# Performance work log

Measured on AMD Instinct MI355X. Metric: run time of the kernel, lower is better.

## Reference

```python
import jax, jax.numpy as jnp
import numpy as np

B, N, F_, H, K_IN, K = 2, 768, 128, 128, 2, 2
TAU = 0.66


def setup_inputs() -> dict:
    key = jax.random.key(0)
    ks = jax.random.split(key, 8)
    s = lambda fan: 1.0 / np.sqrt(fan)
    X = jax.random.normal(ks[0], (B, N, F_), jnp.float32)
    # edge_feat RezeroMLP: Linear(F,H) -> act -> Linear(H,H)
    ef_w1 = jax.random.normal(ks[1], (F_, H), jnp.float32) * s(F_)
    ef_b1 = jnp.zeros((H,), jnp.float32)
    ef_w2 = jax.random.normal(ks[2], (H, H), jnp.float32) * s(H)
    ef_b2 = jnp.zeros((H,), jnp.float32)
    # rezero gate (init 0 in module; use small nonzero so the branch is exercised)
    gate = jnp.asarray(0.1, jnp.float32)
    # score_mlp RezeroMLP: Linear(k_in,H) -> ReLU -> Linear(H,k)
    sm_w1 = jax.random.normal(ks[3], (K_IN, H), jnp.float32) * s(K_IN)
    sm_b1 = jnp.zeros((H,), jnp.float32)
    sm_w2 = jax.random.normal(ks[4], (H, K), jnp.float32) * s(H)
    sm_b2 = jnp.zeros((K,), jnp.float32)
    # pre-sampled standard Gumbel noise for gumbel_softmax
    u = jax.random.uniform(ks[5], (B, N, N, K), jnp.float32, minval=1e-6, maxval=1.0 - 1e-6)
    gumbel = -jnp.log(-jnp.log(u))
    return {"X": X, "ef_w1": ef_w1, "ef_b1": ef_b1, "ef_w2": ef_w2, "ef_b2": ef_b2,
            "gate": gate, "sm_w1": sm_w1, "sm_b1": sm_b1, "sm_w2": sm_w2, "sm_b2": sm_b2,
            "gumbel": gumbel}


def reference(X, ef_w1, ef_b1, ef_w2, ef_b2, gate, sm_w1, sm_b1, sm_w2, sm_b2, gumbel):
    # edge_feat MLP: [B,N,F] -> [B,N,H]
    feats = jax.nn.relu(X @ ef_w1 + ef_b1) @ ef_w2 + ef_b2
    D = H // K_IN
    Xact = feats.reshape(B, N, D, K_IN)
    Xskip = X.reshape(B, N, D, K_IN)  # feat_dim == hidden_dim, proj is None
    Xc = (Xskip + gate * Xact).transpose(0, 3, 1, 2)  # [B,k_in,N,D]
    # pairwise outer product ('prod' scoring): [B,N,N,k_in]
    prod = jnp.einsum('bkid,bkjd->bijk', Xc, Xc)
    # per-edge score MLP: k_in -> H -> k
    scores = jax.nn.relu(prod @ sm_w1 + sm_b1) @ sm_w2 + sm_b2  # [B,N,N,k]
    logits = scores - jnp.max(scores, axis=-1, keepdims=True)
    # gumbel-softmax, hard (straight-through)
    y_soft = jax.nn.softmax((logits + gumbel) / TAU, axis=-1)
    y_hard = jax.nn.one_hot(jnp.argmax(y_soft, axis=-1), K, dtype=y_soft.dtype)
    y = y_hard + y_soft - jax.lax.stop_gradient(y_soft)
    # A = y @ zo with zo = [0,1,...]: probability/one-hot mass of 'edge' states
    zo = jnp.ones((K,), y.dtype).at[0].set(0.0)
    A = y @ zo  # [B,N,N]
    # zero diagonal and symmetrize via upper triangle
    Au = jnp.triu(A, 1)
    return Au + jnp.swapaxes(Au, -1, -2)
```

## Files before the change

### kernel.cpp

```cpp
#include <hip/hip_runtime.h>

#define BB 2
#define NN 768
#define FF 128
#define HH 128
#define TS 32
#define ROWS 8

__global__ void pack_weights_kernel(const float* __restrict__ sm_w1,
                                    const float* __restrict__ sm_b1,
                                    const float* __restrict__ sm_w2,
                                    double* __restrict__ wpack) {
    int c = threadIdx.x;
    if (c < HH) {
        wpack[4 * c + 0] = (double)sm_w1[c];
        wpack[4 * c + 1] = (double)sm_w1[HH + c];
        wpack[4 * c + 2] = (double)sm_b1[c];
        wpack[4 * c + 3] = (double)sm_w2[2 * c + 1] - (double)sm_w2[2 * c + 0];
    }
}

__global__ __launch_bounds__(128)
void edgefeat_kernel(const float* __restrict__ X,
                     const float* __restrict__ w1, const float* __restrict__ b1,
                     const float* __restrict__ w2, const float* __restrict__ b2,
                     const float* __restrict__ gatep,
                     double* __restrict__ Xc) {
    __shared__ float  Xs[ROWS][FF];
    __shared__ double Hs[ROWS][HH];
    const int h = threadIdx.x;
    const int row0 = blockIdx.x * ROWS;
    for (int r = 0; r < ROWS; ++r) Xs[r][h] = X[(size_t)(row0 + r) * FF + h];
    __syncthreads();
    double acc[ROWS];
    double bb = (double)b1[h];
    for (int r = 0; r < ROWS; ++r) acc[r] = bb;
    for (int f = 0; f < FF; ++f) {
        double w = (double)w1[f * HH + h];
        for (int r = 0; r < ROWS; ++r) acc[r] = fma((double)Xs[r][f], w, acc[r]);
    }
    for (int r = 0; r < ROWS; ++r) Hs[r][h] = acc[r] > 0.0 ? acc[r] : 0.0;
    __syncthreads();
    bb = (double)b2[h];
    for (int r = 0; r < ROWS; ++r) acc[r] = bb;
    for (int c = 0; c < HH; ++c) {
        double w = (double)w2[c * HH + h];
        for (int r = 0; r < ROWS; ++r) acc[r] = fma(Hs[r][c], w, acc[r]);
    }
    const double gate = (double)gatep[0];
    const int k = h & 1, d = h >> 1;
    const int b = row0 / NN;
    const int i0 = row0 % NN;
    for (int r = 0; r < ROWS; ++r) {
        double v = (double)Xs[r][h] + gate * acc[r];
        Xc[(((size_t)(b * 2 + k)) * NN + (i0 + r)) * 64 + d] = v;
    }
}

__global__ __launch_bounds__(256, 2)
void edge_decide_kernel(const double* __restrict__ Xc,
                        const double* __restrict__ wpack,
                        const float* __restrict__ sm_b2,
                        const float* __restrict__ gumbel,
                        float* __restrict__ out) {
    const int ti = blockIdx.x, tj = blockIdx.y, b = blockIdx.z;
    if (tj < ti) return;
    __shared__ double Ai[2][TS][66];
    __shared__ double Aj[2][TS][66];
    __shared__ float  As[TS][TS + 1];
    const int tid = threadIdx.x;
    const int i0 = ti * TS, j0 = tj * TS;

    for (int q = 0; q < 8; ++q) {
        int flat = tid + 256 * q;
        int k  = flat >> 10;
        int r  = (flat >> 5) & 31;
        int dp = flat & 31;
        size_t base = ((size_t)(b * 2 + k)) * NN;
        double2 vi = *(const double2*)&Xc[(base + i0 + r) * 64 + 2 * dp];
        *(double2*)&Ai[k][r][2 * dp] = vi;
        double2 vj = *(const double2*)&Xc[(base + j0 + r) * 64 + 2 * dp];
        *(double2*)&Aj[k][r][2 * dp] = vj;
    }
    __syncthreads();

    const int rh = tid >> 4;
    const int ch = tid & 15;
    const int r0 = rh, r1 = rh + 16;
    const int c0 = 2 * ch, c1 = c0 + 1;

    double p000 = 0, p001 = 0, p010 = 0, p011 = 0;
    double p100 = 0, p101 = 0, p110 = 0, p111 = 0;
    for (int d2 = 0; d2 < 32; ++d2) {
        double2 a00 = *(const double2*)&Ai[0][r0][2 * d2];
        double2 a01 = *(const double2*)&Ai[0][r1][2 * d2];
        double2 a10 = *(const double2*)&Ai[1][r0][2 * d2];
        double2 a11 = *(const double2*)&Ai[1][r1][2 * d2];
        double2 b00 = *(const double2*)&Aj[0][c0][2 * d2];
        double2 b01 = *(const double2*)&Aj[0][c1][2 * d2];
        double2 b10 = *(const double2*)&Aj[1][c0][2 * d2];
        double2 b11 = *(const double2*)&Aj[1][c1][2 * d2];
        p000 = fma(a00.y, b00.y, fma(a00.x, b00.x, p000));
        p001 = fma(a00.y, b01.y, fma(a00.x, b01.x, p001));
        p010 = fma(a01.y, b00.y, fma(a01.x, b00.x, p010));
        p011 = fma(a01.y, b01.y, fma(a01.x, b01.x, p011));
        p100 = fma(a10.y, b10.y, fma(a10.x, b10.x, p100));
        p101 = fma(a10.y, b11.y, fma(a10.x, b11.x, p101));
        p110 = fma(a11.y, b10.y, fma(a11.x, b10.x, p110));
        p111 = fma(a11.y, b11.y, fma(a11.x, b11.x, p111));
    }

    const double bd = (double)sm_b2[1] - (double)sm_b2[0];
    float4 g0v = *(const float4*)&gumbel[(((size_t)b * NN + i0 + r0) * NN + j0 + c0) * 2];
    float4 g1v = *(const float4*)&gumbel[(((size_t)b * NN + i0 + r1) * NN + j0 + c0) * 2];
    double m00 = bd + ((double)g0v.y - (double)g0v.x);
    double m01 = bd + ((double)g0v.w - (double)g0v.z);
    double m10 = bd + ((double)g1v.y - (double)g1v.x);
    double m11 = bd + ((double)g1v.w - (double)g1v.z);

    for (int c = 0; c < HH; ++c) {
        double2 wab = *(const double2*)&wpack[4 * c];
        double2 wbw = *(const double2*)&wpack[4 * c + 2];
        double t;
        t = fma(p100, wab.y, fma(p000, wab.x, wbw.x)); t = fmax(t, 0.0); m00 = fma(t, wbw.y, m00);
        t = fma(p101, wab.y, fma(p001, wab.x, wbw.x)); t = fmax(t, 0.0); m01 = fma(t, wbw.y, m01);
        t = fma(p110, wab.y, fma(p010, wab.x, wbw.x)); t = fmax(t, 0.0); m10 = fma(t, wbw.y, m10);
        t = fma(p111, wab.y, fma(p011, wab.x, wbw.x)); t = fmax(t, 0.0); m11 = fma(t, wbw.y, m11);
    }

    float A00 = m00 > 0.0 ? 1.0f : 0.0f;
    float A01 = m01 > 0.0 ? 1.0f : 0.0f;
    float A10 = m10 > 0.0 ? 1.0f : 0.0f;
    float A11 = m11 > 0.0 ? 1.0f : 0.0f;

    As[r0][c0] = A00; As[r0][c1] = A01;
    As[r1][c0] = A10; As[r1][c1] = A11;
    __syncthreads();

    if (ti != tj) {
        *(float2*)&out[((size_t)b * NN + i0 + r0) * NN + j0 + c0] = make_float2(A00, A01);
        *(float2*)&out[((size_t)b * NN + i0 + r1) * NN + j0 + c0] = make_float2(A10, A11);
        float2 t0 = make_float2(As[c0][r0], As[c1][r0]);
        *(float2*)&out[((size_t)b * NN + j0 + r0) * NN + i0 + c0] = t0;
        float2 t1 = make_float2(As[c0][r1], As[c1][r1]);
        *(float2*)&out[((size_t)b * NN + j0 + r1) * NN + i0 + c0] = t1;
    } else {
        float v00 = (r0 < c0) ? As[r0][c0] : ((r0 > c0) ? As[c0][r0] : 0.0f);
        float v01 = (r0 < c1) ? As[r0][c1] : ((r0 > c1) ? As[c1][r0] : 0.0f);
        float v10 = (r1 < c0) ? As[r1][c0] : ((r1 > c0) ? As[c0][r1] : 0.0f);
        float v11 = (r1 < c1) ? As[r1][c1] : ((r1 > c1) ? As[c1][r1] : 0.0f);
        *(float2*)&out[((size_t)b * NN + i0 + r0) * NN + j0 + c0] = make_float2(v00, v01);
        *(float2*)&out[((size_t)b * NN + i0 + r1) * NN + j0 + c0] = make_float2(v10, v11);
    }
}

extern "C" void kernel_launch(void* const* d_in, const int* in_sizes, int n_in,
                              void* d_out, int out_size, void* d_ws, size_t ws_size,
                              hipStream_t stream) {
    const float* X      = (const float*)d_in[0];
    const float* ef_w1  = (const float*)d_in[1];
    const float* ef_b1  = (const float*)d_in[2];
    const float* ef_w2  = (const float*)d_in[3];
    const float* ef_b2  = (const float*)d_in[4];
    const float* gate   = (const float*)d_in[5];
    const float* sm_w1  = (const float*)d_in[6];
    const float* sm_b1  = (const float*)d_in[7];
    const float* sm_w2  = (const float*)d_in[8];
    const float* sm_b2  = (const float*)d_in[9];
    const float* gumbel = (const float*)d_in[10];
    float* out = (float*)d_out;

    double* Xc    = (double*)d_ws;
    double* wpack = Xc + (size_t)BB * 2 * NN * 64;

    pack_weights_kernel<<<1, 128, 0, stream>>>(sm_w1, sm_b1, sm_w2, wpack);
    edgefeat_kernel<<<BB * NN / ROWS, 128, 0, stream>>>(X, ef_w1, ef_b1, ef_w2, ef_b2, gate, Xc);
    dim3 grid(NN / TS, NN / TS, BB);
    edge_decide_kernel<<<grid, 256, 0, stream>>>(Xc, wpack, sm_b2, gumbel, out);
}
```

Baseline: 134.2 us.

## Run score MLP in fp32 with fp64 fallback near decision boundary; fuse weight packing

The per-edge 128-wide score MLP now runs in fp32 from a packed float4 weight table. Only when the fp32 margin falls below a small threshold does it recompute that edge in fp64 through a non-inlined helper. This cuts the dominant fp64 FMA cost while keeping exact hard decisions for near-tie edges. The weight-pack kernel is folded into the edge-feature kernel's first block, removing one launch, and ROWS is halved to give that kernel more blocks. The risk is a wrong decision if fp32 error ever exceeds the threshold, plus divergence cost in the rare fallback path.

```diff
diff --git a/kernel.cpp b/kernel.cpp
--- a/kernel.cpp
+++ b/kernel.cpp
@@ -5,19 +5,27 @@
 #define FF 128
 #define HH 128
 #define TS 32
-#define ROWS 8
-
-__global__ void pack_weights_kernel(const float* __restrict__ sm_w1,
-                                    const float* __restrict__ sm_b1,
-                                    const float* __restrict__ sm_w2,
-                                    double* __restrict__ wpack) {
-    int c = threadIdx.x;
-    if (c < HH) {
-        wpack[4 * c + 0] = (double)sm_w1[c];
-        wpack[4 * c + 1] = (double)sm_w1[HH + c];
-        wpack[4 * c + 2] = (double)sm_b1[c];
-        wpack[4 * c + 3] = (double)sm_w2[2 * c + 1] - (double)sm_w2[2 * c + 0];
-    }
+#define ROWS 4
+#define THR 4e-3f
+
+__device__ __attribute__((noinline))
+double mlp_f64(const double* __restrict__ wpack, double p0, double p1, double m) {
+#pragma unroll 1
+    for (int c = 0; c < HH; ++c) {
+        double2 wab = *(const double2*)&wpack[4 * c];
+        double2 wbw = *(const double2*)&wpack[4 * c + 2];
+        double t = fma(p1, wab.y, fma(p0, wab.x, wbw.x));
+        t = fmax(t, 0.0);
+        m = fma(t, wbw.y, m);
+    }
+    return m;
+}
+
+__device__ inline float decide(float m32, double p0, double p1, double init,
+                               const double* __restrict__ wpack) {
+    if (__builtin_expect(fabsf(m32) < THR, 0))
+        return mlp_f64(wpack, p0, p1, init) > 0.0 ? 1.0f : 0.0f;
+    return m32 > 0.0f ? 1.0f : 0.0f;
 }
 
 __global__ __launch_bounds__(128)
@@ -25,12 +33,27 @@
                      const float* __restrict__ w1, const float* __restrict__ b1,
                      const float* __restrict__ w2, const float* __restrict__ b2,
                      const float* __restrict__ gatep,
-                     double* __restrict__ Xc) {
+                     const float* __restrict__ sm_w1, const float* __restrict__ sm_b1,
+                     const float* __restrict__ sm_w2,
+                     double* __restrict__ Xc,
+                     double* __restrict__ wpack,
+                     float4* __restrict__ wpackf) {
     __shared__ float  Xs[ROWS][FF];
     __shared__ double Hs[ROWS][HH];
     const int h = threadIdx.x;
     const int row0 = blockIdx.x * ROWS;
     for (int r = 0; r < ROWS; ++r) Xs[r][h] = X[(size_t)(row0 + r) * FF + h];
+    if (blockIdx.x == 0) {
+        double a  = (double)sm_w1[h];
+        double bq = (double)sm_w1[HH + h];
+        double be = (double)sm_b1[h];
+        double wd = (double)sm_w2[2 * h + 1] - (double)sm_w2[2 * h + 0];
+        wpack[4 * h + 0] = a;
+        wpack[4 * h + 1] = bq;
+        wpack[4 * h + 2] = be;
+        wpack[4 * h + 3] = wd;
+        wpackf[h] = make_float4((float)a, (float)bq, (float)be, (float)wd);
+    }
     __syncthreads();
     double acc[ROWS];
     double bb = (double)b1[h];
@@ -60,6 +83,7 @@
 __global__ __launch_bounds__(256, 2)
 void edge_decide_kernel(const double* __restrict__ Xc,
                         const double* __restrict__ wpack,
+                        const float4* __restrict__ wpackf,
                         const float* __restrict__ sm_b2,
                         const float* __restrict__ gumbel,
                         float* __restrict__ out) {
@@ -113,25 +137,27 @@
     const double bd = (double)sm_b2[1] - (double)sm_b2[0];
     float4 g0v = *(const float4*)&gumbel[(((size_t)b * NN + i0 + r0) * NN + j0 + c0) * 2];
     float4 g1v = *(const float4*)&gumbel[(((size_t)b * NN + i0 + r1) * NN + j0 + c0) * 2];
-    double m00 = bd + ((double)g0v.y - (double)g0v.x);
-    double m01 = bd + ((double)g0v.w - (double)g0v.z);
-    double m10 = bd + ((double)g1v.y - (double)g1v.x);
-    double m11 = bd + ((double)g1v.w - (double)g1v.z);
-
+    double i00 = bd + ((double)g0v.y - (double)g0v.x);
+    double i01 = bd + ((double)g0v.w - (double)g0v.z);
+    double i10 = bd + ((double)g1v.y - (double)g1v.x);
+    double i11 = bd + ((double)g1v.w - (double)g1v.z);
+
+    float m00 = (float)i00, m01 = (float)i01, m10 = (float)i10, m11 = (float)i11;
+    float q000 = (float)p000, q001 = (float)p001, q010 = (float)p010, q011 = (float)p011;
+    float q100 = (float)p100, q101 = (float)p101, q110 = (float)p110, q111 = (float)p111;
     for (int c = 0; c < HH; ++c) {
-        double2 wab = *(const double2*)&wpack[4 * c];
-        double2 wbw = *(const double2*)&wpack[4 * c + 2];
-        double t;
-        t = fma(p100, wab.y, fma(p000, wab.x, wbw.x)); t = fmax(t, 0.0); m00 = fma(t, wbw.y, m00);
-        t = fma(p101, wab.y, fma(p001, wab.x, wbw.x)); t = fmax(t, 0.0); m01 = fma(t, wbw.y, m01);
-        t = fma(p110, wab.y, fma(p010, wab.x, wbw.x)); t = fmax(t, 0.0); m10 = fma(t, wbw.y, m10);
-        t = fma(p111, wab.y, fma(p011, wab.x, wbw.x)); t = fmax(t, 0.0); m11 = fma(t, wbw.y, m11);
-    }
-
-    float A00 = m00 > 0.0 ? 1.0f : 0.0f;
-    float A01 = m01 > 0.0 ? 1.0f : 0.0f;
-    float A10 = m10 > 0.0 ? 1.0f : 0.0f;
-    float A11 = m11 > 0.0 ? 1.0f : 0.0f;
+        float4 wf = wpackf[c];
+        float t;
+        t = fmaf(q100, wf.y, fmaf(q000, wf.x, wf.z)); t = fmaxf(t, 0.0f); m00 = fmaf(t, wf.w, m00);
+        t = fmaf(q101, wf.y, fmaf(q001, wf.x, wf.z)); t = fmaxf(t, 0.0f); m01 = fmaf(t, wf.w, m01);
+        t = fmaf(q110, wf.y, fmaf(q010, wf.x, wf.z)); t = fmaxf(t, 0.0f); m10 = fmaf(t, wf.w, m10);
+        t = fmaf(q111, wf.y, fmaf(q011, wf.x, wf.z)); t = fmaxf(t, 0.0f); m11 = fmaf(t, wf.w, m11);
+    }
+
+    float A00 = decide(m00, p000, p100, i00, wpack);
+    float A01 = decide(m01, p001, p101, i01, wpack);
+    float A10 = decide(m10, p010, p110, i10, wpack);
+    float A11 = decide(m11, p011, p111, i11, wpack);
 
     As[r0][c0] = A00; As[r0][c1] = A01;
     As[r1][c0] = A10; As[r1][c1] = A11;
@@ -170,11 +196,12 @@
     const float* gumbel = (const float*)d_in[10];
     float* out = (float*)d_out;
 
-    double* Xc    = (double*)d_ws;
-    double* wpack = Xc + (size_t)BB * 2 * NN * 64;
-
-    pack_weights_kernel<<<1, 128, 0, stream>>>(sm_w1, sm_b1, sm_w2, wpack);
-    edgefeat_kernel<<<BB * NN / ROWS, 128, 0, stream>>>(X, ef_w1, ef_b1, ef_w2, ef_b2, gate, Xc);
+    double* Xc     = (double*)d_ws;
+    double* wpack  = Xc + (size_t)BB * 2 * NN * 64;
+    float4* wpackf = (float4*)(wpack + 4 * HH);
+
+    edgefeat_kernel<<<BB * NN / ROWS, 128, 0, stream>>>(
+        X, ef_w1, ef_b1, ef_w2, ef_b2, gate, sm_w1, sm_b1, sm_w2, Xc, wpack, wpackf);
     dim3 grid(NN / TS, NN / TS, BB);
-    edge_decide_kernel<<<grid, 256, 0, stream>>>(Xc, wpack, sm_b2, gumbel, out);
-}
+    edge_decide_kernel<<<grid, 256, 0, stream>>>(Xc, wpack, wpackf, sm_b2, gumbel, out);
+}
```

Result: slower. 152.2 us (+13.4%).
